# Optimization experiments

Measured on AMD Instinct MI355X. Metric: run time of the kernel, lower is better.

Reference implementation:

```python
import jax, jax.numpy as jnp
import numpy as np

B, N, C = 16, 2048, 128
NCLS = 40


def setup_inputs() -> dict:
    key = jax.random.key(0)
    ks = iter(jax.random.split(key, 40))

    def nrm(shape, s=0.05):
        return jax.random.normal(next(ks), shape, dtype=jnp.float32) * s

    return {
        "x": jax.random.normal(next(ks), (B, 3, N), dtype=jnp.float32),
        "conv1_w": nrm((128, 3), 0.5),
        "bn1_g": jnp.ones((128,), jnp.float32), "bn1_b": jnp.zeros((128,), jnp.float32),
        "conv2_w": nrm((128, 128)),
        "bn2_g": jnp.ones((128,), jnp.float32), "bn2_b": jnp.zeros((128,), jnp.float32),
        "sa_wqk": nrm((4, 32, 128)),
        "sa_wv": nrm((4, 128, 128)), "sa_bv": nrm((4, 128)),
        "sa_wt": nrm((4, 128, 128)), "sa_bt": nrm((4, 128)),
        "sa_g": jnp.ones((4, 128), jnp.float32), "sa_b": jnp.zeros((4, 128), jnp.float32),
        "fuse_w": nrm((1024, 512)),
        "fuse_g": jnp.ones((1024,), jnp.float32), "fuse_b": jnp.zeros((1024,), jnp.float32),
        "lin1_w": nrm((512, 1024)),
        "bn6_g": jnp.ones((512,), jnp.float32), "bn6_b": jnp.zeros((512,), jnp.float32),
        "lin2_w": nrm((256, 512)), "lin2_b": jnp.zeros((256,), jnp.float32),
        "bn7_g": jnp.ones((256,), jnp.float32), "bn7_b": jnp.zeros((256,), jnp.float32),
        "lin3_w": nrm((NCLS, 256)), "lin3_b": jnp.zeros((NCLS,), jnp.float32),
    }


def _pconv(w, x):
    # 1x1 Conv1d == channel matmul: [O,C] x [B,C,N] -> [B,O,N]
    return jnp.einsum('oc,bcn->bon', w, x)


def _fwd(x, conv1_w, bn1_g, bn1_b, conv2_w, bn2_g, bn2_b,
         sa_wqk, sa_wv, sa_bv, sa_wt, sa_bt, sa_g, sa_b,
         fuse_w, fuse_g, fuse_b, lin1_w, bn6_g, bn6_b,
         lin2_w, lin2_b, bn7_g, bn7_b, lin3_w, lin3_b):
    # conv stem (BN in eval mode: running mean=0, var=1 -> affine)
    h = jax.nn.relu(bn1_g[:, None] * _pconv(conv1_w, x) + bn1_b[:, None])
    h = jax.nn.relu(bn2_g[:, None] * _pconv(conv2_w, h) + bn2_b[:, None])

    outs = []
    for i in range(4):  # fixed number of structurally identical SA blocks
        # q_conv and k_conv share the same weight (aliased in the torch code)
        q = jnp.einsum('dc,bcn->bdn', sa_wqk[i], h)           # [B,32,N]
        energy = jnp.einsum('bdi,bdj->bij', q, q)             # [B,N,N]
        att = jax.nn.softmax(energy, axis=-1)
        att = att / (1e-9 + att.sum(axis=1, keepdims=True))   # extra L1 renorm over dim=1
        v = _pconv(sa_wv[i], h) + sa_bv[i][:, None]           # [B,C,N]
        x_r = jnp.einsum('bcn,bnm->bcm', v, att)              # [B,C,N]
        t = _pconv(sa_wt[i], h - x_r) + sa_bt[i][:, None]
        h = h + jax.nn.relu(sa_g[i][:, None] * t + sa_b[i][:, None])
        outs.append(h)

    cat = jnp.concatenate(outs, axis=1)                        # [B,512,N]
    f = fuse_g[:, None] * _pconv(fuse_w, cat) + fuse_b[:, None]
    f = jnp.where(f > 0, f, 0.2 * f)                           # LeakyReLU(0.2)
    g = f.max(axis=-1)                                         # adaptive max pool -> [B,1024]

    h1 = jax.nn.relu(bn6_g * (g @ lin1_w.T) + bn6_b)           # dropout = identity (eval)
    h2 = jax.nn.relu(bn7_g * (h1 @ lin2_w.T + lin2_b) + bn7_b)
    return h2 @ lin3_w.T + lin3_b                              # [B,40]


def reference(x, conv1_w, bn1_g, bn1_b, conv2_w, bn2_g, bn2_b,
              sa_wqk, sa_wv, sa_bv, sa_wt, sa_bt, sa_g, sa_b,
              fuse_w, fuse_g, fuse_b, lin1_w, bn6_g, bn6_b,
              lin2_w, lin2_b, bn7_g, bn7_b, lin3_w, lin3_b):
    return _fwd(x, conv1_w, bn1_g, bn1_b, conv2_w, bn2_g, bn2_b,
                sa_wqk, sa_wv, sa_bv, sa_wt, sa_bt, sa_g, sa_b,
                fuse_w, fuse_g, fuse_b, lin1_w, bn6_g, bn6_b,
                lin2_w, lin2_b, bn7_g, bn7_b, lin3_w, lin3_b)
```

## Files before the change

kernel.cpp:

```cpp
#include <hip/hip_runtime.h>

typedef __attribute__((ext_vector_type(4))) float f4;
typedef __attribute__((ext_vector_type(8))) short s16x8;
typedef __attribute__((ext_vector_type(4))) unsigned short us4;
typedef __attribute__((ext_vector_type(2))) unsigned int u32x2;
typedef unsigned short u16;
typedef unsigned int u32;

#define DEVI __device__ __forceinline__

DEVI u16 f2bf(float f){
    u32 u = __builtin_bit_cast(u32, f);
    u32 r = (u + 0x7fffu + ((u >> 16) & 1u)) >> 16;
    return (u16)r;
}
DEVI f4 mfma16(s16x8 a, s16x8 b, f4 c){
    return __builtin_amdgcn_mfma_f32_16x16x32_bf16(a, b, c, 0, 0, 0);
}
DEVI u32 cvtpk(float lo, float hi){
    u32 r;
    asm("v_cvt_pk_bf16_f32 %0, %1, %2" : "=v"(r) : "v"(lo), "v"(hi));
    return r;
}
DEVI void gload(const u16* g, u16* l){
    __builtin_amdgcn_global_load_lds((const __attribute__((address_space(1))) void*)g,
                                     (__attribute__((address_space(3))) void*)l, 16, 0, 0);
}

#define L2E 1.44269504088896340736f

__global__ __launch_bounds__(256) void k_cast(const float* w2, const float* wqk,
                                              const float* wv, const float* wt,
                                              const float* wf, u16* out){
    int i = blockIdx.x * 256 + threadIdx.x;
    if(i < 16384)       out[i] = f2bf(w2[i]);
    else if(i < 32768)  out[i] = f2bf(wqk[i - 16384]);
    else if(i < 98304)  out[i] = f2bf(wv[i - 32768]);
    else if(i < 163840) out[i] = f2bf(wt[i - 98304]);
    else if(i < 688128){
        int t = i - 163840;
        int o = t >> 9, c = t & 511;
        int jg = o >> 4, l15 = o & 15, ks = c >> 5, kr = c & 31;
        out[163840 + (size_t)(jg*16 + ks)*512 + ((kr>>3)*16 + l15)*8 + (kr&7)] = f2bf(wf[t]);
    }
}

__global__ __launch_bounds__(256) void k_stem1(const float* x, const float* w1,
                                               const float* g1, const float* b1, u16* h1tb){
    int t = blockIdx.x * 256 + threadIdx.x;
    int b = t >> 11, n = t & 2047;
    const float* xb = x + (size_t)b * 3 * 2048 + n;
    float x0 = xb[0], x1 = xb[2048], x2 = xb[4096];
    u32* o = (u32*)(h1tb + (size_t)t * 128);
    #pragma unroll 8
    for(int c = 0; c < 128; c += 2){
        float a0 = fmaxf(g1[c]   * (w1[c*3+0]*x0 + w1[c*3+1]*x1 + w1[c*3+2]*x2) + b1[c],   0.f);
        float a1 = fmaxf(g1[c+1] * (w1[c*3+3]*x0 + w1[c*3+4]*x1 + w1[c*3+5]*x2) + b1[c+1], 0.f);
        o[c >> 1] = (u32)f2bf(a0) | ((u32)f2bf(a1) << 16);
    }
}

DEVI int swz512(int bid){ return ((bid & 7) << 6) | (bid >> 3); }
DEVI int swz1024(int bid){ return ((bid & 7) << 7) | (bid >> 3); }

DEVI void qv_phase(const u16* T, const u16* wqkb, const u16* wvb, const float* bv,
                   u16* qb, u16* vt, int b, int n0, int wv_, int l15, int kg){
    f4 accv[8], accq[2];
    #pragma unroll
    for(int j=0;j<8;j++) accv[j] = (f4){0.f,0.f,0.f,0.f};
    accq[0] = (f4){0.f,0.f,0.f,0.f}; accq[1] = accq[0];
    int row = wv_*16 + l15;
    #pragma unroll
    for(int ks=0; ks<4; ks++){
        s16x8 a = *(const s16x8*)&T[row*128 + ((ks*32 + kg*8) ^ ((row&7)<<3))];
        #pragma unroll
        for(int j=0;j<8;j++){
            s16x8 bb = *(const s16x8*)(wvb + (size_t)(j*16 + l15)*128 + ks*32 + kg*8);
            accv[j] = mfma16(a, bb, accv[j]);
        }
        #pragma unroll
        for(int f=0; f<2; f++){
            s16x8 wf_ = *(const s16x8*)(wqkb + (size_t)(f*16 + l15)*128 + ks*32 + kg*8);
            accq[f] = mfma16(wf_, a, accq[f]);
        }
    }
    int nb = n0 + wv_*16;
    int it = nb >> 5;
    int k0 = (nb & 31) + kg*4;
    int vbase = ((k0 >> 3)*16)*8 + (k0 & 7);
    #pragma unroll
    for(int j=0;j<8;j++){
        float bvo = bv[j*16 + l15];
        us4 pk;
        #pragma unroll
        for(int r=0;r<4;r++) pk[r] = f2bf(accv[j][r] + bvo);
        *(us4*)(vt + (size_t)((b*64 + it)*8 + j)*512 + vbase + l15*8) = pk;
    }
    int n = n0 + wv_*16 + l15;
    #pragma unroll
    for(int f=0; f<2; f++){
        us4 pk;
        #pragma unroll
        for(int r=0;r<4;r++) pk[r] = f2bf(accq[f][r]);
        *(us4*)(qb + (size_t)(b*2048 + n)*32 + f*16 + kg*4) = pk;
    }
}

__global__ __launch_bounds__(256) void k_conv2qv(const u16* h1tb, const u16* w2b,
                                                 const float* g2, const float* b2,
                                                 float* ht0,
                                                 const u16* wqkb, const u16* wvb,
                                                 const float* bv, u16* qb, u16* vt){
    __shared__ u16 T[8192];
    int bid2 = swz512(blockIdx.x);
    int b = bid2 >> 5;
    int n0 = (bid2 & 31) << 6;
    int lane = threadIdx.x & 63, wv_ = threadIdx.x >> 6;
    int l15 = lane & 15, kg = lane >> 4;
    const u16* arow = h1tb + (size_t)(b*2048 + n0 + wv_*16 + l15) * 128 + kg*8;
    f4 acc[8];
    #pragma unroll
    for(int j=0;j<8;j++) acc[j] = (f4){0.f,0.f,0.f,0.f};
    #pragma unroll
    for(int ks=0; ks<4; ks++){
        s16x8 a = *(const s16x8*)(arow + ks*32);
        #pragma unroll
        for(int j=0;j<8;j++){
            s16x8 bb = *(const s16x8*)(w2b + (size_t)(j*16 + l15)*128 + ks*32 + kg*8);
            acc[j] = mfma16(a, bb, acc[j]);
        }
    }
    int nn0 = n0 + wv_*16 + kg*4;
    #pragma unroll
    for(int j=0;j<8;j++){
        int o = j*16 + l15;
        float gg = g2[o], be = b2[o];
        #pragma unroll
        for(int r=0;r<4;r++){
            float h = fmaxf(gg * acc[j][r] + be, 0.f);
            int nl = wv_*16 + kg*4 + r;
            ht0[(size_t)(b*2048 + nn0 + r) * 128 + o] = h;
            T[nl*128 + (o ^ ((nl&7)<<3))] = f2bf(h);
        }
    }
    __syncthreads();
    qv_phase(T, wqkb, wvb, bv, qb, vt, b, n0, wv_, l15, kg);
}

__global__ __launch_bounds__(256) void k_passA(const u16* qb, float* crowp){
    int bid2 = swz1024(blockIdx.x);
    int b = bid2 >> 6;
    int rest = bid2 & 63;
    int i0 = (rest >> 1) << 6;
    int jh = rest & 1;
    int jbeg = jh << 10;
    int lane = threadIdx.x & 63, wv_ = threadIdx.x >> 6;
    int l15 = lane & 15, kg = lane >> 4;
    const u16* qbase = qb + (size_t)b * 2048 * 32;
    s16x8 af = *(const s16x8*)(qbase + (size_t)(i0 + wv_*16 + l15)*32 + kg*8);
    float m[4], s[4], mml[4];
    const f4 z = {0.f,0.f,0.f,0.f};
    {
        s16x8 b0 = *(const s16x8*)(qbase + (size_t)(jbeg + l15)*32 + kg*8);
        s16x8 b1 = *(const s16x8*)(qbase + (size_t)(jbeg + 16 + l15)*32 + kg*8);
        f4 e0 = mfma16(af, b0, z);
        f4 e1 = mfma16(af, b1, z);
        #pragma unroll
        for(int r=0;r<4;r++){
            m[r] = fmaxf(e0[r], e1[r]);
            mml[r] = -m[r]*L2E;
            s[r] = exp2f(fmaf(e0[r], L2E, mml[r])) + exp2f(fmaf(e1[r], L2E, mml[r]));
        }
    }
    for(int j0=jbeg+32; j0<jbeg+1024; j0+=32){
        s16x8 b0 = *(const s16x8*)(qbase + (size_t)(j0 + l15)*32 + kg*8);
        s16x8 b1 = *(const s16x8*)(qbase + (size_t)(j0 + 16 + l15)*32 + kg*8);
        f4 e0 = mfma16(af, b0, z);
        f4 e1 = mfma16(af, b1, z);
        #pragma unroll
        for(int r=0;r<4;r++){
            float mx = fmaxf(e0[r], e1[r]);
            if(mx > m[r] + 8.f){
                s[r] *= exp2f((m[r]-mx)*L2E);
                m[r] = mx; mml[r] = -mx*L2E;
            }
            s[r] += exp2f(fmaf(e0[r], L2E, mml[r])) + exp2f(fmaf(e1[r], L2E, mml[r]));
        }
    }
    #pragma unroll
    for(int d=1; d<16; d<<=1){
        #pragma unroll
        for(int r=0;r<4;r++){
            float mo = __shfl_xor(m[r], d);
            float so = __shfl_xor(s[r], d);
            float mn = fmaxf(m[r], mo);
            s[r] = s[r]*exp2f((m[r]-mn)*L2E) + so*exp2f((mo-mn)*L2E);
            m[r] = mn;
        }
    }
    if(l15 == 0){
        #pragma unroll
        for(int r=0;r<4;r++){
            int i = i0 + wv_*16 + kg*4 + r;
            crowp[jh*32768 + b*2048 + i] = m[r]*L2E + log2f(s[r]);
        }
    }
}

__global__ __launch_bounds__(512) void k_passBT(const u16* qb, const u16* vt,
                                                const float* crowp,
                                                const float* hprev, int ldh,
                                                const u16* wtb, const float* bt,
                                                const float* sg, const float* sb,
                                                float* catf_o, u16* catb_o,
                                                const u16* wqkb2, const u16* wvb2,
                                                const float* bv2,
                                                u16* qb2, u16* vt2, int doQV){
    __shared__ __align__(16) char SB[49664];
    u16*   V   = (u16*)SB;
    u16*   P   = (u16*)(SB + 32768);
    float* CR  = (float*)(SB + 40960);
    float* csl = (float*)(SB + 49152);
    int bid2 = swz512(blockIdx.x);
    int b = bid2 >> 5;
    int j0 = (bid2 & 31) << 6;
    int tid = threadIdx.x;
    int lane = tid & 63, wv_ = tid >> 6;
    int jw = wv_ >> 1, ih = wv_ & 1;
    int l15 = lane & 15, kg = lane >> 4;
    int jh = jw * 16;
    const u16* qbase = qb + (size_t)b * 2048 * 32;
    const u16* vtb = vt + (size_t)b * 64*8*512;

    #pragma unroll
    for(int p=0;p<4;p++){
        int i = p*512 + tid;
        float c0 = crowp[b*2048 + i], c1 = crowp[32768 + b*2048 + i];
        float mx = fmaxf(c0, c1), mn = fminf(c0, c1);
        CR[i] = mx + log2f(1.f + exp2f(mn - mx));
    }

    s16x8 eb = *(const s16x8*)(qbase + (size_t)(j0 + jh + l15)*32 + kg*8);
    f4 acc[8];
    #pragma unroll
    for(int j=0;j<8;j++) acc[j] = (f4){0.f,0.f,0.f,0.f};
    float csp = 0.f;
    const f4 z = {0.f,0.f,0.f,0.f};

    auto stage = [&](int ic, int buf){
        const u16* src = vtb + (size_t)ic*8192 + wv_*1024 + lane*8;
        u16* dst = V + buf*8192 + wv_*1024;
        gload(src, dst);
        gload(src + 512, dst + 512);
    };
    auto eph = [&](int ic){
        #pragma unroll
        for(int is=0; is<2; is++){
            int isub = ih*2 + is;
            s16x8 ea = *(const s16x8*)(qbase + (size_t)(ic*64 + isub*16 + l15)*32 + kg*8);
            f4 e = mfma16(ea, eb, z);
            f4 cc = *(const f4*)&CR[ic*64 + isub*16 + kg*4];
            float q0 = exp2f(fmaf(e[0], L2E, -cc[0]));
            float q1 = exp2f(fmaf(e[1], L2E, -cc[1]));
            float q2 = exp2f(fmaf(e[2], L2E, -cc[2]));
            float q3 = exp2f(fmaf(e[3], L2E, -cc[3]));
            csp += q0 + q1 + q2 + q3;
            u32x2 pk = { cvtpk(q0, q1), cvtpk(q2, q3) };
            int idx = wv_*512 + ((is*2 + (kg>>1))*16 + l15)*8 + (kg&1)*4;
            *(u32x2*)&P[idx] = pk;
        }
    };

    __syncthreads();
    stage(0, 0);
    eph(0);
    __syncthreads();
    for(int it=0; it<32; it++){
        int cur = it & 1;
        s16x8 pa = *(const s16x8*)&P[wv_*512 + lane*8];
        if(it < 31){ stage(it+1, cur^1); eph(it+1); }
        __builtin_amdgcn_s_setprio(1);
        #pragma unroll
        for(int jc=0;jc<8;jc++){
            s16x8 vf = *(const s16x8*)&V[cur*8192 + ih*4096 + jc*512 + lane*8];
            acc[jc] = mfma16(pa, vf, acc[jc]);
        }
        __builtin_amdgcn_s_setprio(0);
        __syncthreads();
    }
    csp += __shfl_xor(csp, 16);
    csp += __shfl_xor(csp, 32);
    if(lane < 16) csl[ih*64 + jh + l15] = csp;
    __syncthreads();
    float* comb = (float*)SB;
    if(ih == 1){
        #pragma unroll
        for(int jc=0;jc<8;jc++)
            *(f4*)&comb[jw*2048 + jc*256 + lane*4] = acc[jc];
    }
    __syncthreads();
    u16* Td = (u16*)(SB + 32768);
    if(ih == 0){
        #pragma unroll
        for(int jc=0;jc<8;jc++){
            f4 o = *(const f4*)&comb[jw*2048 + jc*256 + lane*4];
            acc[jc][0] += o[0]; acc[jc][1] += o[1];
            acc[jc][2] += o[2]; acc[jc][3] += o[3];
        }
        #pragma unroll
        for(int r=0;r<4;r++){
            int jr = jh + kg*4 + r;
            float inv = 1.0f / (1e-9f + csl[jr] + csl[64 + jr]);
            int n = j0 + jr;
            const float* hrow = hprev + (size_t)(b*2048 + n)*ldh;
            #pragma unroll
            for(int jc=0;jc<8;jc++){
                int c = jc*16 + l15;
                Td[jr*128 + (c ^ ((jr&7)<<3))] = f2bf(hrow[c] - acc[jc][r]*inv);
            }
        }
    }
    __syncthreads();
    f4 accT[4];
    #pragma unroll
    for(int j2=0;j2<4;j2++) accT[j2] = (f4){0.f,0.f,0.f,0.f};
    {
        int arow_l = jh + l15;
        #pragma unroll
        for(int ks=0; ks<4; ks++){
            s16x8 a = *(const s16x8*)&Td[arow_l*128 + ((ks*32 + kg*8) ^ ((arow_l&7)<<3))];
            #pragma unroll
            for(int j2=0;j2<4;j2++){
                int o = ih*64 + j2*16 + l15;
                s16x8 bb = *(const s16x8*)(wtb + (size_t)o*128 + ks*32 + kg*8);
                accT[j2] = mfma16(a, bb, accT[j2]);
            }
        }
    }
    u16* T2 = (u16*)SB;
    #pragma unroll
    for(int j2=0;j2<4;j2++){
        int o = ih*64 + j2*16 + l15;
        float bto = bt[o], gg = sg[o], be = sb[o];
        #pragma unroll
        for(int r=0;r<4;r++){
            int jr = jh + kg*4 + r;
            int n = j0 + jr;
            float t = accT[j2][r] + bto;
            float hv = hprev[(size_t)(b*2048 + n)*ldh + o];
            float hn = hv + fmaxf(gg*t + be, 0.f);
            size_t oi = (size_t)(b*2048 + n)*512 + o;
            u16 hb = f2bf(hn);
            catf_o[oi] = hn;
            catb_o[oi] = hb;
            T2[jr*128 + (o ^ ((jr&7)<<3))] = hb;
        }
    }
    __syncthreads();
    if(doQV){
        f4 accv[4], accq;
        #pragma unroll
        for(int jj=0;jj<4;jj++) accv[jj] = (f4){0.f,0.f,0.f,0.f};
        accq = (f4){0.f,0.f,0.f,0.f};
        int row = jh + l15;
        #pragma unroll
        for(int ks=0; ks<4; ks++){
            s16x8 a = *(const s16x8*)&T2[row*128 + ((ks*32 + kg*8) ^ ((row&7)<<3))];
            #pragma unroll
            for(int jj=0;jj<4;jj++){
                s16x8 bb = *(const s16x8*)(wvb2 + (size_t)((ih*4+jj)*16 + l15)*128 + ks*32 + kg*8);
                accv[jj] = mfma16(a, bb, accv[jj]);
            }
            s16x8 wf_ = *(const s16x8*)(wqkb2 + (size_t)(ih*16 + l15)*128 + ks*32 + kg*8);
            accq = mfma16(wf_, a, accq);
        }
        int nb = j0 + jh;
        int it2 = nb >> 5;
        int k0 = (nb & 31) + kg*4;
        int vbase = ((k0 >> 3)*16)*8 + (k0 & 7);
        #pragma unroll
        for(int jj=0;jj<4;jj++){
            int jc4 = ih*4 + jj;
            float bvo = bv2[jc4*16 + l15];
            us4 pk;
            #pragma unroll
            for(int r=0;r<4;r++) pk[r] = f2bf(accv[jj][r] + bvo);
            *(us4*)(vt2 + (size_t)((b*64 + it2)*8 + jc4)*512 + vbase + l15*8) = pk;
        }
        int n = j0 + jh + l15;
        us4 pk;
        #pragma unroll
        for(int r=0;r<4;r++) pk[r] = f2bf(accq[r]);
        *(us4*)(qb2 + (size_t)(b*2048 + n)*32 + ih*16 + kg*4) = pk;
    }
}

__global__ __launch_bounds__(512) void k_fuse(const u16* catb, const u16* wft,
                                              const float* fg, const float* fb, float* gpart){
    __shared__ u16 AB[24576];
    __shared__ float red[512];
    int bid2 = swz1024(blockIdx.x);
    int b  = bid2 >> 6;
    int rest = bid2 & 63;
    int ng = rest >> 2;
    int og = rest & 3;
    int tid = threadIdx.x;
    int lane = tid & 63, wv_ = tid >> 6;
    int wn = wv_ >> 2, wo = wv_ & 3;
    int l15 = lane & 15, kg = lane >> 4;

    f4 acc[4][4];
    #pragma unroll
    for(int mi=0;mi<4;mi++)
        #pragma unroll
        for(int j=0;j<4;j++) acc[mi][j] = (f4){0.f,0.f,0.f,0.f};

    for(int ksc=0; ksc<8; ksc++){
        if(ksc) __syncthreads();
        #pragma unroll
        for(int q=0;q<2;q++){
            int s = wv_*128 + q*64 + lane;
            int r = s >> 3;
            int c16 = (s & 7) ^ (r & 7);
            const u16* g = catb + (size_t)(b*2048 + ng*128 + r)*512 + ksc*64 + c16*8;
            gload(g, &AB[wv_*1024 + q*512]);
        }
        #pragma unroll
        for(int q=0;q<4;q++){
            int p = wv_*4 + q;
            int jgl = p >> 1, ksl = p & 1;
            const u16* g = wft + (size_t)((og*16 + jgl)*16 + ksc*2 + ksl)*512 + lane*8;
            gload(g, &AB[8192 + p*512]);
        }
        __syncthreads();
        #pragma unroll
        for(int ks=0; ks<2; ks++){
            s16x8 av[4], bw[4];
            #pragma unroll
            for(int mi=0;mi<4;mi++){
                int row = wn*64 + mi*16 + l15;
                av[mi] = *(const s16x8*)&AB[row*64 + ((ks*32 + kg*8) ^ ((row&7)<<3))];
            }
            #pragma unroll
            for(int j=0;j<4;j++){
                int p = (wo*4 + j)*2 + ks;
                bw[j] = *(const s16x8*)&AB[8192 + p*512 + lane*8];
            }
            #pragma unroll
            for(int j=0;j<4;j++)
                #pragma unroll
                for(int mi=0;mi<4;mi++)
                    acc[mi][j] = mfma16(av[mi], bw[j], acc[mi][j]);
        }
    }
    float vmax[4];
    #pragma unroll
    for(int j=0;j<4;j++){
        int o = og*256 + wo*64 + j*16 + l15;
        float fgv = fg[o], fbv = fb[o];
        float vm = -1e30f;
        #pragma unroll
        for(int mi=0;mi<4;mi++)
            #pragma unroll
            for(int r=0;r<4;r++){
                float f = fgv*acc[mi][j][r] + fbv;
                f = (f > 0.f) ? f : 0.2f*f;
                vm = fmaxf(vm, f);
            }
        vm = fmaxf(vm, __shfl_xor(vm, 16));
        vm = fmaxf(vm, __shfl_xor(vm, 32));
        vmax[j] = vm;
    }
    if(lane < 16){
        #pragma unroll
        for(int j=0;j<4;j++) red[(wo*2 + wn)*64 + j*16 + lane] = vmax[j];
    }
    __syncthreads();
    if(tid < 256){
        int wo2 = tid >> 6, ol = tid & 63;
        float m = fmaxf(red[(wo2*2+0)*64 + ol], red[(wo2*2+1)*64 + ol]);
        gpart[(size_t)(ng*16 + b)*1024 + og*256 + wo2*64 + ol] = m;
    }
}

__global__ __launch_bounds__(256) void k_gmax(const float* gpart, float* g){
    int i = blockIdx.x*256 + threadIdx.x;
    float m = gpart[i];
    #pragma unroll
    for(int p=1;p<16;p++) m = fmaxf(m, gpart[(size_t)p*16384 + i]);
    g[i] = m;
}

__global__ __launch_bounds__(256) void k_mlp(const float* in, const float* W, const float* bias,
                                             const float* gm, const float* bt, float* out,
                                             int IN, int OUT, int dorelu){
    int wid = blockIdx.x*4 + (threadIdx.x >> 6);
    int lane = threadIdx.x & 63;
    int b = wid / OUT, o = wid - b*OUT;
    if(b >= 16) return;
    const f4* ir = (const f4*)(in + (size_t)b*IN);
    const f4* wr = (const f4*)(W + (size_t)o*IN);
    float s = 0.f;
    for(int k=lane; k < (IN>>2); k += 64){
        f4 a = ir[k], w = wr[k];
        s += a[0]*w[0] + a[1]*w[1] + a[2]*w[2] + a[3]*w[3];
    }
    #pragma unroll
    for(int d=1; d<64; d<<=1) s += __shfl_xor(s, d);
    if(lane == 0){
        if(bias) s += bias[o];
        if(gm) s = gm[o]*s + bt[o];
        if(dorelu) s = fmaxf(s, 0.f);
        out[(size_t)b*OUT + o] = s;
    }
}

constexpr size_t MB = 1048576;
constexpr size_t OFF_WB   = 0;
constexpr size_t OFF_H1TB = 2*MB;
constexpr size_t OFF_HT0  = 10*MB;
constexpr size_t OFF_QB0  = 26*MB;
constexpr size_t OFF_QB1  = 28*MB;
constexpr size_t OFF_VB0  = 30*MB;
constexpr size_t OFF_VB1  = 38*MB;
constexpr size_t OFF_CROW = 46*MB;
constexpr size_t OFF_GP   = 46*MB + 262144;
constexpr size_t OFF_CATF = 48*MB;
constexpr size_t OFF_CATB = 112*MB;
constexpr size_t OFF_G    = 144*MB;
constexpr size_t OFF_H1V  = OFF_G + 65536;
constexpr size_t OFF_H2V  = OFF_H1V + 32768;

extern "C" void kernel_launch(void* const* d_in, const int* in_sizes, int n_in,
                              void* d_out, int out_size, void* d_ws, size_t ws_size,
                              hipStream_t stream){
    const float* x       = (const float*)d_in[0];
    const float* conv1_w = (const float*)d_in[1];
    const float* bn1_g   = (const float*)d_in[2];
    const float* bn1_b   = (const float*)d_in[3];
    const float* conv2_w = (const float*)d_in[4];
    const float* bn2_g   = (const float*)d_in[5];
    const float* bn2_b   = (const float*)d_in[6];
    const float* sa_wqk  = (const float*)d_in[7];
    const float* sa_wv   = (const float*)d_in[8];
    const float* sa_bv   = (const float*)d_in[9];
    const float* sa_wt   = (const float*)d_in[10];
    const float* sa_bt   = (const float*)d_in[11];
    const float* sa_g    = (const float*)d_in[12];
    const float* sa_b    = (const float*)d_in[13];
    const float* fuse_w  = (const float*)d_in[14];
    const float* fuse_g  = (const float*)d_in[15];
    const float* fuse_b  = (const float*)d_in[16];
    const float* lin1_w  = (const float*)d_in[17];
    const float* bn6_g   = (const float*)d_in[18];
    const float* bn6_b   = (const float*)d_in[19];
    const float* lin2_w  = (const float*)d_in[20];
    const float* lin2_b  = (const float*)d_in[21];
    const float* bn7_g   = (const float*)d_in[22];
    const float* bn7_b   = (const float*)d_in[23];
    const float* lin3_w  = (const float*)d_in[24];
    const float* lin3_b  = (const float*)d_in[25];

    char* ws = (char*)d_ws;
    u16*   wb    = (u16*)(ws + OFF_WB);
    u16*   h1tb  = (u16*)(ws + OFF_H1TB);
    float* ht0   = (float*)(ws + OFF_HT0);
    u16*   qbb[2] = { (u16*)(ws + OFF_QB0), (u16*)(ws + OFF_QB1) };
    u16*   vtb[2] = { (u16*)(ws + OFF_VB0), (u16*)(ws + OFF_VB1) };
    float* crowp = (float*)(ws + OFF_CROW);
    float* gpart = (float*)(ws + OFF_GP);
    float* catf  = (float*)(ws + OFF_CATF);
    u16*   catb  = (u16*)(ws + OFF_CATB);
    float* gbuf  = (float*)(ws + OFF_G);
    float* h1v   = (float*)(ws + OFF_H1V);
    float* h2v   = (float*)(ws + OFF_H2V);

    k_cast <<<2688, 256, 0, stream>>>(conv2_w, sa_wqk, sa_wv, sa_wt, fuse_w, wb);
    k_stem1<<<128,  256, 0, stream>>>(x, conv1_w, bn1_g, bn1_b, h1tb);
    k_conv2qv<<<512, 256, 0, stream>>>(h1tb, wb, bn2_g, bn2_b, ht0,
                                       wb + 16384, wb + 32768, sa_bv, qbb[0], vtb[0]);

    for(int blk = 0; blk < 4; blk++){
        int cur = blk & 1, nxt = cur ^ 1;
        const float* hprev = (blk == 0) ? ht0 : (catf + (size_t)(blk-1)*128);
        int          ldh   = (blk == 0) ? 128 : 512;
        const u16* wtb  = wb + 98304 + blk*16384;
        int nb2 = (blk < 3) ? (blk + 1) : 3;
        const u16* wqkb2 = wb + 16384 + nb2*4096;
        const u16* wvb2  = wb + 32768 + nb2*16384;

        k_passA<<<1024, 256, 0, stream>>>(qbb[cur], crowp);
        k_passBT<<<512, 512, 0, stream>>>(qbb[cur], vtb[cur], crowp, hprev, ldh,
                                          wtb, sa_bt + blk*128, sa_g + blk*128, sa_b + blk*128,
                                          catf + (size_t)blk*128, catb + (size_t)blk*128,
                                          wqkb2, wvb2, sa_bv + nb2*128,
                                          qbb[nxt], vtb[nxt], (blk < 3) ? 1 : 0);
    }

    k_fuse<<<1024, 512, 0, stream>>>(catb, wb + 163840, fuse_g, fuse_b, gpart);
    k_gmax<<<64,   256, 0, stream>>>(gpart, gbuf);
    k_mlp <<<2048, 256, 0, stream>>>(gbuf, lin1_w, nullptr, bn6_g, bn6_b, h1v, 1024, 512, 1);
    k_mlp <<<1024, 256, 0, stream>>>(h1v, lin2_w, lin2_b, bn7_g, bn7_b, h2v, 512, 256, 1);
    k_mlp <<<160,  256, 0, stream>>>(h2v, lin3_w, lin3_b, nullptr, nullptr,
                                     (float*)d_out, 256, 40, 0);
}
```

Baseline: 460.0 us.

## Retile attention PV pass so each wave computes 32 rows and double-buffer P

Changes the k_passBT wave decomposition in the attention-times-V loop. Each wave now owns 32 query rows and half of the value columns, so every V fragment read from shared memory feeds two MFMAs and each energy A-fragment is reused across two row blocks. P is now double-buffered, which lets the next tile's probabilities be written before the current tile is consumed, and row sums are split into four partial groups. The cost is more shared memory (about 57 KB per block), which may lower occupancy, plus extra register use for the doubled accumulators.

```diff
diff --git a/kernel.cpp b/kernel.cpp
--- a/kernel.cpp
+++ b/kernel.cpp
@@ -216,19 +216,21 @@
                                                 const u16* wqkb2, const u16* wvb2,
                                                 const float* bv2,
                                                 u16* qb2, u16* vt2, int doQV){
-    __shared__ __align__(16) char SB[49664];
+    __shared__ __align__(16) char SB[58368];
     u16*   V   = (u16*)SB;
     u16*   P   = (u16*)(SB + 32768);
-    float* CR  = (float*)(SB + 40960);
-    float* csl = (float*)(SB + 49152);
+    float* CR  = (float*)(SB + 49152);
+    float* csl = (float*)(SB + 57344);
     int bid2 = swz512(blockIdx.x);
     int b = bid2 >> 5;
     int j0 = (bid2 & 31) << 6;
     int tid = threadIdx.x;
     int lane = tid & 63, wv_ = tid >> 6;
-    int jw = wv_ >> 1, ih = wv_ & 1;
+    int jw = wv_ >> 2, ih = (wv_ >> 1) & 1, jcH = wv_ & 1;
     int l15 = lane & 15, kg = lane >> 4;
-    int jh = jw * 16;
+    int jh = jw * 32;
+    int pairOff = (jw*2 + ih) * 1024;
+    int isub = ih*2 + jcH;
     const u16* qbase = qb + (size_t)b * 2048 * 32;
     const u16* vtb = vt + (size_t)b * 64*8*512;
 
@@ -240,11 +242,14 @@
         CR[i] = mx + log2f(1.f + exp2f(mn - mx));
     }
 
-    s16x8 eb = *(const s16x8*)(qbase + (size_t)(j0 + jh + l15)*32 + kg*8);
-    f4 acc[8];
-    #pragma unroll
-    for(int j=0;j<8;j++) acc[j] = (f4){0.f,0.f,0.f,0.f};
-    float csp = 0.f;
+    s16x8 eb0 = *(const s16x8*)(qbase + (size_t)(j0 + jh + l15)*32 + kg*8);
+    s16x8 eb1 = *(const s16x8*)(qbase + (size_t)(j0 + jh + 16 + l15)*32 + kg*8);
+    f4 acc[2][4];
+    #pragma unroll
+    for(int jb=0;jb<2;jb++)
+        #pragma unroll
+        for(int jj=0;jj<4;jj++) acc[jb][jj] = (f4){0.f,0.f,0.f,0.f};
+    float csp0 = 0.f, csp1 = 0.f;
     const f4 z = {0.f,0.f,0.f,0.f};
 
     auto stage = [&](int ic, int buf){
@@ -253,85 +258,107 @@
         gload(src, dst);
         gload(src + 512, dst + 512);
     };
-    auto eph = [&](int ic){
-        #pragma unroll
-        for(int is=0; is<2; is++){
-            int isub = ih*2 + is;
-            s16x8 ea = *(const s16x8*)(qbase + (size_t)(ic*64 + isub*16 + l15)*32 + kg*8);
-            f4 e = mfma16(ea, eb, z);
-            f4 cc = *(const f4*)&CR[ic*64 + isub*16 + kg*4];
+    auto eph = [&](int ic, int buf){
+        s16x8 ea = *(const s16x8*)(qbase + (size_t)(ic*64 + isub*16 + l15)*32 + kg*8);
+        f4 cc = *(const f4*)&CR[ic*64 + isub*16 + kg*4];
+        int wbase = buf*4096 + pairOff + ((jcH*2 + (kg>>1))*16 + l15)*8 + (kg&1)*4;
+        {
+            f4 e = mfma16(ea, eb0, z);
             float q0 = exp2f(fmaf(e[0], L2E, -cc[0]));
             float q1 = exp2f(fmaf(e[1], L2E, -cc[1]));
             float q2 = exp2f(fmaf(e[2], L2E, -cc[2]));
             float q3 = exp2f(fmaf(e[3], L2E, -cc[3]));
-            csp += q0 + q1 + q2 + q3;
+            csp0 += q0 + q1 + q2 + q3;
             u32x2 pk = { cvtpk(q0, q1), cvtpk(q2, q3) };
-            int idx = wv_*512 + ((is*2 + (kg>>1))*16 + l15)*8 + (kg&1)*4;
-            *(u32x2*)&P[idx] = pk;
+            *(u32x2*)&P[wbase] = pk;
+        }
+        {
+            f4 e = mfma16(ea, eb1, z);
+            float q0 = exp2f(fmaf(e[0], L2E, -cc[0]));
+            float q1 = exp2f(fmaf(e[1], L2E, -cc[1]));
+            float q2 = exp2f(fmaf(e[2], L2E, -cc[2]));
+            float q3 = exp2f(fmaf(e[3], L2E, -cc[3]));
+            csp1 += q0 + q1 + q2 + q3;
+            u32x2 pk = { cvtpk(q0, q1), cvtpk(q2, q3) };
+            *(u32x2*)&P[wbase + 512] = pk;
         }
     };
 
     __syncthreads();
     stage(0, 0);
-    eph(0);
+    eph(0, 0);
     __syncthreads();
     for(int it=0; it<32; it++){
         int cur = it & 1;
-        s16x8 pa = *(const s16x8*)&P[wv_*512 + lane*8];
-        if(it < 31){ stage(it+1, cur^1); eph(it+1); }
+        if(it < 31){ stage(it+1, cur^1); eph(it+1, cur^1); }
+        s16x8 pa0 = *(const s16x8*)&P[cur*4096 + pairOff + lane*8];
+        s16x8 pa1 = *(const s16x8*)&P[cur*4096 + pairOff + 512 + lane*8];
         __builtin_amdgcn_s_setprio(1);
         #pragma unroll
-        for(int jc=0;jc<8;jc++){
-            s16x8 vf = *(const s16x8*)&V[cur*8192 + ih*4096 + jc*512 + lane*8];
-            acc[jc] = mfma16(pa, vf, acc[jc]);
+        for(int jj=0;jj<4;jj++){
+            s16x8 vf = *(const s16x8*)&V[cur*8192 + ih*4096 + (jcH*4 + jj)*512 + lane*8];
+            acc[0][jj] = mfma16(pa0, vf, acc[0][jj]);
+            acc[1][jj] = mfma16(pa1, vf, acc[1][jj]);
         }
         __builtin_amdgcn_s_setprio(0);
         __syncthreads();
     }
-    csp += __shfl_xor(csp, 16);
-    csp += __shfl_xor(csp, 32);
-    if(lane < 16) csl[ih*64 + jh + l15] = csp;
+    csp0 += __shfl_xor(csp0, 16); csp0 += __shfl_xor(csp0, 32);
+    csp1 += __shfl_xor(csp1, 16); csp1 += __shfl_xor(csp1, 32);
+    if(lane < 16){
+        int g = ih*2 + jcH;
+        csl[g*64 + jh + l15]      = csp0;
+        csl[g*64 + jh + 16 + l15] = csp1;
+    }
     __syncthreads();
     float* comb = (float*)SB;
     if(ih == 1){
         #pragma unroll
-        for(int jc=0;jc<8;jc++)
-            *(f4*)&comb[jw*2048 + jc*256 + lane*4] = acc[jc];
+        for(int jb=0;jb<2;jb++)
+            #pragma unroll
+            for(int jj=0;jj<4;jj++)
+                *(f4*)&comb[(jw*2+jcH)*2048 + (jb*4+jj)*256 + lane*4] = acc[jb][jj];
     }
     __syncthreads();
     u16* Td = (u16*)(SB + 32768);
     if(ih == 0){
         #pragma unroll
-        for(int jc=0;jc<8;jc++){
-            f4 o = *(const f4*)&comb[jw*2048 + jc*256 + lane*4];
-            acc[jc][0] += o[0]; acc[jc][1] += o[1];
-            acc[jc][2] += o[2]; acc[jc][3] += o[3];
-        }
-        #pragma unroll
-        for(int r=0;r<4;r++){
-            int jr = jh + kg*4 + r;
-            float inv = 1.0f / (1e-9f + csl[jr] + csl[64 + jr]);
-            int n = j0 + jr;
-            const float* hrow = hprev + (size_t)(b*2048 + n)*ldh;
-            #pragma unroll
-            for(int jc=0;jc<8;jc++){
-                int c = jc*16 + l15;
-                Td[jr*128 + (c ^ ((jr&7)<<3))] = f2bf(hrow[c] - acc[jc][r]*inv);
-            }
-        }
-    }
-    __syncthreads();
+        for(int jb=0;jb<2;jb++)
+            #pragma unroll
+            for(int jj=0;jj<4;jj++){
+                f4 o = *(const f4*)&comb[(jw*2+jcH)*2048 + (jb*4+jj)*256 + lane*4];
+                acc[jb][jj][0] += o[0]; acc[jb][jj][1] += o[1];
+                acc[jb][jj][2] += o[2]; acc[jb][jj][3] += o[3];
+            }
+        #pragma unroll
+        for(int jb=0;jb<2;jb++)
+            #pragma unroll
+            for(int r=0;r<4;r++){
+                int jr = jh + jb*16 + kg*4 + r;
+                float inv = 1.0f / (1e-9f + csl[jr] + csl[64+jr] + csl[128+jr] + csl[192+jr]);
+                int n = j0 + jr;
+                const float* hrow = hprev + (size_t)(b*2048 + n)*ldh;
+                #pragma unroll
+                for(int jj=0;jj<4;jj++){
+                    int c = (jcH*4 + jj)*16 + l15;
+                    Td[jr*128 + (c ^ ((jr&7)<<3))] = f2bf(hrow[c] - acc[jb][jj][r]*inv);
+                }
+            }
+    }
+    __syncthreads();
+    int jw2 = wv_ >> 1, ih2 = wv_ & 1;
+    int jh2 = jw2 * 16;
     f4 accT[4];
     #pragma unroll
     for(int j2=0;j2<4;j2++) accT[j2] = (f4){0.f,0.f,0.f,0.f};
     {
-        int arow_l = jh + l15;
+        int arow_l = jh2 + l15;
         #pragma unroll
         for(int ks=0; ks<4; ks++){
             s16x8 a = *(const s16x8*)&Td[arow_l*128 + ((ks*32 + kg*8) ^ ((arow_l&7)<<3))];
             #pragma unroll
             for(int j2=0;j2<4;j2++){
-                int o = ih*64 + j2*16 + l15;
+                int o = ih2*64 + j2*16 + l15;
                 s16x8 bb = *(const s16x8*)(wtb + (size_t)o*128 + ks*32 + kg*8);
                 accT[j2] = mfma16(a, bb, accT[j2]);
             }
@@ -340,11 +367,11 @@
     u16* T2 = (u16*)SB;
     #pragma unroll
     for(int j2=0;j2<4;j2++){
-        int o = ih*64 + j2*16 + l15;
+        int o = ih2*64 + j2*16 + l15;
         float bto = bt[o], gg = sg[o], be = sb[o];
         #pragma unroll
         for(int r=0;r<4;r++){
-            int jr = jh + kg*4 + r;
+            int jr = jh2 + kg*4 + r;
             int n = j0 + jr;
             float t = accT[j2][r] + bto;
             float hv = hprev[(size_t)(b*2048 + n)*ldh + o];
@@ -362,36 +389,36 @@
         #pragma unroll
         for(int jj=0;jj<4;jj++) accv[jj] = (f4){0.f,0.f,0.f,0.f};
         accq = (f4){0.f,0.f,0.f,0.f};
-        int row = jh + l15;
+        int row = jh2 + l15;
         #pragma unroll
         for(int ks=0; ks<4; ks++){
             s16x8 a = *(const s16x8*)&T2[row*128 + ((ks*32 + kg*8) ^ ((row&7)<<3))];
             #pragma unroll
             for(int jj=0;jj<4;jj++){
-                s16x8 bb = *(const s16x8*)(wvb2 + (size_t)((ih*4+jj)*16 + l15)*128 + ks*32 + kg*8);
+                s16x8 bb = *(const s16x8*)(wvb2 + (size_t)((ih2*4+jj)*16 + l15)*128 + ks*32 + kg*8);
                 accv[jj] = mfma16(a, bb, accv[jj]);
             }
-            s16x8 wf_ = *(const s16x8*)(wqkb2 + (size_t)(ih*16 + l15)*128 + ks*32 + kg*8);
+            s16x8 wf_ = *(const s16x8*)(wqkb2 + (size_t)(ih2*16 + l15)*128 + ks*32 + kg*8);
             accq = mfma16(wf_, a, accq);
         }
-        int nb = j0 + jh;
+        int nb = j0 + jh2;
         int it2 = nb >> 5;
         int k0 = (nb & 31) + kg*4;
         int vbase = ((k0 >> 3)*16)*8 + (k0 & 7);
         #pragma unroll
         for(int jj=0;jj<4;jj++){
-            int jc4 = ih*4 + jj;
+            int jc4 = ih2*4 + jj;
             float bvo = bv2[jc4*16 + l15];
             us4 pk;
             #pragma unroll
             for(int r=0;r<4;r++) pk[r] = f2bf(accv[jj][r] + bvo);
             *(us4*)(vt2 + (size_t)((b*64 + it2)*8 + jc4)*512 + vbase + l15*8) = pk;
         }
-        int n = j0 + jh + l15;
+        int n = j0 + jh2 + l15;
         us4 pk;
         #pragma unroll
         for(int r=0;r<4;r++) pk[r] = f2bf(accq[r]);
-        *(us4*)(qb2 + (size_t)(b*2048 + n)*32 + ih*16 + kg*4) = pk;
+        *(us4*)(qb2 + (size_t)(b*2048 + n)*32 + ih2*16 + kg*4) = pk;
     }
 }
 
```

Result: faster. 448.7 us, median of 3 (-2.4%).

## Halve passBT tile to 32 columns, precompute row normalizers in a separate kernel

Applied to the files above, without the earlier changes.

The attention pass-B kernel now uses 256-thread blocks that each own 32 query columns instead of 64, doubling the grid to 1024 blocks. The per-row log-sum-exp combine moves into a small k_comb kernel, so each block reads precombined constants from global memory instead of recomputing all 2048 of them into shared memory. Together with the smaller shared-memory footprint this aims at more resident blocks and better latency hiding. The cost is an extra launch per SA block and twice as many blocks that each restream the full V tiles, which doubles V traffic through L2.

```diff
diff --git a/kernel.cpp b/kernel.cpp
--- a/kernel.cpp
+++ b/kernel.cpp
@@ -207,8 +207,15 @@
     }
 }
 
-__global__ __launch_bounds__(512) void k_passBT(const u16* qb, const u16* vt,
-                                                const float* crowp,
+__global__ __launch_bounds__(256) void k_comb(const float* crowp, float* crg){
+    int i = blockIdx.x*256 + threadIdx.x;
+    float c0 = crowp[i], c1 = crowp[32768 + i];
+    float mx = fmaxf(c0, c1), mn = fminf(c0, c1);
+    crg[i] = mx + log2f(1.f + exp2f(mn - mx));
+}
+
+__global__ __launch_bounds__(256) void k_passBT(const u16* qb, const u16* vt,
+                                                const float* crg,
                                                 const float* hprev, int ldh,
                                                 const u16* wtb, const float* bt,
                                                 const float* sg, const float* sb,
@@ -216,14 +223,13 @@
                                                 const u16* wqkb2, const u16* wvb2,
                                                 const float* bv2,
                                                 u16* qb2, u16* vt2, int doQV){
-    __shared__ __align__(16) char SB[49664];
+    __shared__ __align__(16) char SB[37120];
     u16*   V   = (u16*)SB;
     u16*   P   = (u16*)(SB + 32768);
-    float* CR  = (float*)(SB + 40960);
-    float* csl = (float*)(SB + 49152);
-    int bid2 = swz512(blockIdx.x);
-    int b = bid2 >> 5;
-    int j0 = (bid2 & 31) << 6;
+    float* csl = (float*)(SB + 36864);
+    int bid2 = swz1024(blockIdx.x);
+    int b = bid2 >> 6;
+    int j0 = (bid2 & 63) << 5;
     int tid = threadIdx.x;
     int lane = tid & 63, wv_ = tid >> 6;
     int jw = wv_ >> 1, ih = wv_ & 1;
@@ -231,14 +237,7 @@
     int jh = jw * 16;
     const u16* qbase = qb + (size_t)b * 2048 * 32;
     const u16* vtb = vt + (size_t)b * 64*8*512;
-
-    #pragma unroll
-    for(int p=0;p<4;p++){
-        int i = p*512 + tid;
-        float c0 = crowp[b*2048 + i], c1 = crowp[32768 + b*2048 + i];
-        float mx = fmaxf(c0, c1), mn = fminf(c0, c1);
-        CR[i] = mx + log2f(1.f + exp2f(mn - mx));
-    }
+    const float* cb = crg + b * 2048;
 
     s16x8 eb = *(const s16x8*)(qbase + (size_t)(j0 + jh + l15)*32 + kg*8);
     f4 acc[8];
@@ -248,10 +247,10 @@
     const f4 z = {0.f,0.f,0.f,0.f};
 
     auto stage = [&](int ic, int buf){
-        const u16* src = vtb + (size_t)ic*8192 + wv_*1024 + lane*8;
-        u16* dst = V + buf*8192 + wv_*1024;
-        gload(src, dst);
-        gload(src + 512, dst + 512);
+        const u16* src = vtb + (size_t)ic*8192 + wv_*2048 + lane*8;
+        u16* dst = V + buf*8192 + wv_*2048;
+        #pragma unroll
+        for(int p=0;p<4;p++) gload(src + p*512, dst + p*512);
     };
     auto eph = [&](int ic){
         #pragma unroll
@@ -259,7 +258,7 @@
             int isub = ih*2 + is;
             s16x8 ea = *(const s16x8*)(qbase + (size_t)(ic*64 + isub*16 + l15)*32 + kg*8);
             f4 e = mfma16(ea, eb, z);
-            f4 cc = *(const f4*)&CR[ic*64 + isub*16 + kg*4];
+            f4 cc = *(const f4*)(cb + ic*64 + isub*16 + kg*4);
             float q0 = exp2f(fmaf(e[0], L2E, -cc[0]));
             float q1 = exp2f(fmaf(e[1], L2E, -cc[1]));
             float q2 = exp2f(fmaf(e[2], L2E, -cc[2]));
@@ -271,7 +270,6 @@
         }
     };
 
-    __syncthreads();
     stage(0, 0);
     eph(0);
     __syncthreads();
@@ -290,16 +288,15 @@
     }
     csp += __shfl_xor(csp, 16);
     csp += __shfl_xor(csp, 32);
-    if(lane < 16) csl[ih*64 + jh + l15] = csp;
-    __syncthreads();
     float* comb = (float*)SB;
+    if(lane < 16) csl[ih*32 + jh + l15] = csp;
     if(ih == 1){
         #pragma unroll
         for(int jc=0;jc<8;jc++)
             *(f4*)&comb[jw*2048 + jc*256 + lane*4] = acc[jc];
     }
     __syncthreads();
-    u16* Td = (u16*)(SB + 32768);
+    u16* Td = (u16*)(SB + 16384);
     if(ih == 0){
         #pragma unroll
         for(int jc=0;jc<8;jc++){
@@ -310,7 +307,7 @@
         #pragma unroll
         for(int r=0;r<4;r++){
             int jr = jh + kg*4 + r;
-            float inv = 1.0f / (1e-9f + csl[jr] + csl[64 + jr]);
+            float inv = 1.0f / (1e-9f + csl[jr] + csl[32 + jr]);
             int n = j0 + jr;
             const float* hrow = hprev + (size_t)(b*2048 + n)*ldh;
             #pragma unroll
@@ -321,30 +318,32 @@
         }
     }
     __syncthreads();
+    int jw2 = wv_ >> 1, ih2 = wv_ & 1;
+    int jh2 = jw2 * 16;
     f4 accT[4];
     #pragma unroll
     for(int j2=0;j2<4;j2++) accT[j2] = (f4){0.f,0.f,0.f,0.f};
     {
-        int arow_l = jh + l15;
+        int arow_l = jh2 + l15;
         #pragma unroll
         for(int ks=0; ks<4; ks++){
             s16x8 a = *(const s16x8*)&Td[arow_l*128 + ((ks*32 + kg*8) ^ ((arow_l&7)<<3))];
             #pragma unroll
             for(int j2=0;j2<4;j2++){
-                int o = ih*64 + j2*16 + l15;
+                int o = ih2*64 + j2*16 + l15;
                 s16x8 bb = *(const s16x8*)(wtb + (size_t)o*128 + ks*32 + kg*8);
                 accT[j2] = mfma16(a, bb, accT[j2]);
             }
         }
     }
-    u16* T2 = (u16*)SB;
+    u16* T2 = (u16*)(SB + 24576);
     #pragma unroll
     for(int j2=0;j2<4;j2++){
-        int o = ih*64 + j2*16 + l15;
+        int o = ih2*64 + j2*16 + l15;
         float bto = bt[o], gg = sg[o], be = sb[o];
         #pragma unroll
         for(int r=0;r<4;r++){
-            int jr = jh + kg*4 + r;
+            int jr = jh2 + kg*4 + r;
             int n = j0 + jr;
             float t = accT[j2][r] + bto;
             float hv = hprev[(size_t)(b*2048 + n)*ldh + o];
@@ -362,36 +361,36 @@
         #pragma unroll
         for(int jj=0;jj<4;jj++) accv[jj] = (f4){0.f,0.f,0.f,0.f};
         accq = (f4){0.f,0.f,0.f,0.f};
-        int row = jh + l15;
+        int row = jh2 + l15;
         #pragma unroll
         for(int ks=0; ks<4; ks++){
             s16x8 a = *(const s16x8*)&T2[row*128 + ((ks*32 + kg*8) ^ ((row&7)<<3))];
             #pragma unroll
             for(int jj=0;jj<4;jj++){
-                s16x8 bb = *(const s16x8*)(wvb2 + (size_t)((ih*4+jj)*16 + l15)*128 + ks*32 + kg*8);
+                s16x8 bb = *(const s16x8*)(wvb2 + (size_t)((ih2*4+jj)*16 + l15)*128 + ks*32 + kg*8);
                 accv[jj] = mfma16(a, bb, accv[jj]);
             }
-            s16x8 wf_ = *(const s16x8*)(wqkb2 + (size_t)(ih*16 + l15)*128 + ks*32 + kg*8);
+            s16x8 wf_ = *(const s16x8*)(wqkb2 + (size_t)(ih2*16 + l15)*128 + ks*32 + kg*8);
             accq = mfma16(wf_, a, accq);
         }
-        int nb = j0 + jh;
+        int nb = j0 + jh2;
         int it2 = nb >> 5;
         int k0 = (nb & 31) + kg*4;
         int vbase = ((k0 >> 3)*16)*8 + (k0 & 7);
         #pragma unroll
         for(int jj=0;jj<4;jj++){
-            int jc4 = ih*4 + jj;
+            int jc4 = ih2*4 + jj;
             float bvo = bv2[jc4*16 + l15];
             us4 pk;
             #pragma unroll
             for(int r=0;r<4;r++) pk[r] = f2bf(accv[jj][r] + bvo);
             *(us4*)(vt2 + (size_t)((b*64 + it2)*8 + jc4)*512 + vbase + l15*8) = pk;
         }
-        int n = j0 + jh + l15;
+        int n = j0 + jh2 + l15;
         us4 pk;
         #pragma unroll
         for(int r=0;r<4;r++) pk[r] = f2bf(accq[r]);
-        *(us4*)(qb2 + (size_t)(b*2048 + n)*32 + ih*16 + kg*4) = pk;
+        *(us4*)(qb2 + (size_t)(b*2048 + n)*32 + ih2*16 + kg*4) = pk;
     }
 }
 
@@ -524,7 +523,8 @@
 constexpr size_t OFF_VB0  = 30*MB;
 constexpr size_t OFF_VB1  = 38*MB;
 constexpr size_t OFF_CROW = 46*MB;
-constexpr size_t OFF_GP   = 46*MB + 262144;
+constexpr size_t OFF_CRG  = 46*MB + 262144;
+constexpr size_t OFF_GP   = OFF_CRG + 131072;
 constexpr size_t OFF_CATF = 48*MB;
 constexpr size_t OFF_CATB = 112*MB;
 constexpr size_t OFF_G    = 144*MB;
@@ -568,6 +568,7 @@
     u16*   qbb[2] = { (u16*)(ws + OFF_QB0), (u16*)(ws + OFF_QB1) };
     u16*   vtb[2] = { (u16*)(ws + OFF_VB0), (u16*)(ws + OFF_VB1) };
     float* crowp = (float*)(ws + OFF_CROW);
+    float* crg   = (float*)(ws + OFF_CRG);
     float* gpart = (float*)(ws + OFF_GP);
     float* catf  = (float*)(ws + OFF_CATF);
     u16*   catb  = (u16*)(ws + OFF_CATB);
@@ -590,11 +591,12 @@
         const u16* wvb2  = wb + 32768 + nb2*16384;
 
         k_passA<<<1024, 256, 0, stream>>>(qbb[cur], crowp);
-        k_passBT<<<512, 512, 0, stream>>>(qbb[cur], vtb[cur], crowp, hprev, ldh,
-                                          wtb, sa_bt + blk*128, sa_g + blk*128, sa_b + blk*128,
-                                          catf + (size_t)blk*128, catb + (size_t)blk*128,
-                                          wqkb2, wvb2, sa_bv + nb2*128,
-                                          qbb[nxt], vtb[nxt], (blk < 3) ? 1 : 0);
+        k_comb <<<128,  256, 0, stream>>>(crowp, crg);
+        k_passBT<<<1024, 256, 0, stream>>>(qbb[cur], vtb[cur], crg, hprev, ldh,
+                                           wtb, sa_bt + blk*128, sa_g + blk*128, sa_b + blk*128,
+                                           catf + (size_t)blk*128, catb + (size_t)blk*128,
+                                           wqkb2, wvb2, sa_bv + nb2*128,
+                                           qbb[nxt], vtb[nxt], (blk < 3) ? 1 : 0);
     }
 
     k_fuse<<<1024, 512, 0, stream>>>(catb, wb + 163840, fuse_g, fuse_b, gpart);
```

After: 538.5 us. +17.1%, slower.
